# Kernel optimization log

Measured on AMD Instinct MI355X. Metric: run time of the kernel, lower is better.

## Reference

```python
import jax, jax.numpy as jnp
import numpy as np

B, H, W = 8, 448, 448
NUM_CLASSES, NUM_FEATURES = 80, 1280
TOPN, THRESHOLD = 4, 0.5


def conv(x, w, b, stride, pad):
    y = jax.lax.conv_general_dilated(x, w, (stride, stride), [(pad, pad), (pad, pad)],
                                     dimension_numbers=('NCHW', 'OIHW', 'NCHW'))
    return y + b[None, :, None, None]


def sample_bilinear(img, ys, xs):
    # img: [C, Hs, Ws]; ys: [oh] float coords; xs: [ow] float coords (align_corners=True grid)
    Hs, Ws = img.shape[1], img.shape[2]
    y0 = jnp.clip(jnp.floor(ys), 0.0, Hs - 1.0)
    x0 = jnp.clip(jnp.floor(xs), 0.0, Ws - 1.0)
    y0i = y0.astype(jnp.int32); y1i = jnp.minimum(y0i + 1, Hs - 1)
    x0i = x0.astype(jnp.int32); x1i = jnp.minimum(x0i + 1, Ws - 1)
    wy = (ys - y0)[:, None]   # [oh,1]
    wx = (xs - x0)[None, :]   # [1,ow]
    r0 = img[:, y0i, :]; r1 = img[:, y1i, :]          # [C,oh,Ws]
    a = r0[:, :, x0i]; b_ = r0[:, :, x1i]             # [C,oh,ow]
    c = r1[:, :, x0i]; d = r1[:, :, x1i]
    top = a * (1.0 - wx) + b_ * wx
    bot = c * (1.0 - wx) + d * wx
    return top * (1.0 - wy) + bot * wy


def minmax_norm(s):
    # torch: if max==min: s/max else (s-min)/(max-min); sigmoid output so max>0
    mn = s.min(-1, keepdims=True); mx = s.max(-1, keepdims=True)
    rng = mx - mn
    return jnp.where(rng > 0, (s - mn) / jnp.where(rng > 0, rng, 1.0),
                     s / jnp.where(mx != 0, mx, 1.0))


def obj_loc(score, threshold, dim):
    # first/last threshold crossing with min-size fallback (vectorized over leading dims)
    mask = score >= threshold
    any_ = mask.any(-1)
    first = jnp.argmax(mask, axis=-1)
    last = dim - jnp.argmax(mask[..., ::-1], axis=-1)   # exclusive
    lo = jnp.where(any_, first, int(dim * 0.125)).astype(jnp.int32)
    hi = jnp.where(any_, last, int(dim * 0.875)).astype(jnp.int32)
    minsize = int(np.ceil(dim * 0.125))
    need = jnp.maximum(minsize - (hi - lo), 0)
    lo = jnp.maximum(lo - (need + 1) // 2, 0)
    hi = jnp.minimum(hi + (need + 1) // 2, dim)
    return lo, hi


def one_crop(img, y1, y2, x1, x2):
    # crop img[:, y1:y2, x1:x2] and bilinearly resize to (H,W), align_corners=True
    oh, ow = img.shape[1], img.shape[2]
    ys = y1.astype(jnp.float32) + jnp.arange(oh, dtype=jnp.float32) * ((y2 - 1 - y1).astype(jnp.float32) / (oh - 1))
    xs = x1.astype(jnp.float32) + jnp.arange(ow, dtype=jnp.float32) * ((x2 - 1 - x1).astype(jnp.float32) / (ow - 1))
    return sample_bilinear(img, ys, xs)


def setup_inputs() -> dict:
    key = jax.random.key(0)
    k1, k2, k3 = jax.random.split(key, 3)
    return {
        'inputs': jax.random.normal(k1, (B, 3, H, W), dtype=jnp.float32),
        'feat_w': jax.random.normal(k2, (NUM_FEATURES, 3, 3, 3), dtype=jnp.float32) * 0.05,
        'feat_b': jnp.zeros((NUM_FEATURES,), dtype=jnp.float32),
        'cls_w': jax.random.normal(k3, (NUM_CLASSES, NUM_FEATURES, 1, 1), dtype=jnp.float32) * 0.02,
        'cls_b': jnp.zeros((NUM_CLASSES,), dtype=jnp.float32),
    }


def reference(inputs, feat_w, feat_b, cls_w, cls_b):
    b, c, h, w = inputs.shape
    # ---- backbone (stride-32 stand-in for MobileNetV2 features) ----
    ga = jnp.clip(conv(inputs, feat_w, feat_b, 32, 1), 0.0, 6.0)     # [b,1280,h/32,w/32]
    gf = ga.mean((2, 3), keepdims=True)                               # avg pool sh=h/32
    gs = jax.nn.sigmoid(conv(gf, cls_w, cls_b, 1, 0)).reshape(b, -1)  # [b,num_classes]
    # ---- CAM score path (on detached ga) ----
    cam = jax.nn.sigmoid(conv(jax.lax.stop_gradient(ga), cls_w, cls_b, 1, 0))
    ys_g = jnp.linspace(0.0, cam.shape[2] - 1.0, h)
    xs_g = jnp.linspace(0.0, cam.shape[3] - 1.0, w)
    cam_up = jax.vmap(lambda im: sample_bilinear(im, ys_g, xs_g))(cam)  # [b,C,h,w]
    wscore = cam_up.max(axis=2)   # max over height -> [b,C,w]
    hscore = cam_up.max(axis=3)   # max over width  -> [b,C,h]
    # ---- topN classes by global score ----
    _, topi = jax.lax.top_k(gs, TOPN)                                  # [b,topN]
    xs_s = jnp.take_along_axis(wscore, topi[:, :, None], axis=1)       # [b,topN,w]
    ys_s = jnp.take_along_axis(hscore, topi[:, :, None], axis=1)       # [b,topN,h]
    x1, x2 = obj_loc(minmax_norm(xs_s), THRESHOLD, w)
    y1, y2 = obj_loc(minmax_norm(ys_s), THRESHOLD, h)
    # ---- dynamic crop + bilinear resize, vectorized over (b, topN) ----
    crops = jax.vmap(lambda img, a1, a2, b1, b2:
                     jax.vmap(lambda p, q, r, s: one_crop(img, p, q, r, s))(a1, a2, b1, b2)
                     )(inputs, y1, y2, x1, x2)                          # [b,topN,3,h,w]
    li = jax.lax.stop_gradient(crops.reshape(b * TOPN, 3, h, w))
    la = jnp.clip(conv(li, feat_w, feat_b, 32, 1), 0.0, 6.0)
    lf = la.mean((2, 3), keepdims=True)
    ls = jax.nn.sigmoid(conv(lf, cls_w, cls_b, 1, 0)).reshape(b, TOPN, -1).max(axis=1)
    return gs, ls
```

## Files before the change

kernel.cpp:

```cpp
#include <hip/hip_runtime.h>
#include <math.h>

#define NB 8
#define TOPN 4
#define NC 80
#define NF 1280
#define HW 448
#define OS 14
#define NP 196
#define PATCH (3*42*42)
#define ROWPATCH (3*3*42)
#define WLDS (256*27)

__device__ __forceinline__ float sigmoidf_(float x) { return 1.0f / (1.0f + expf(-x)); }

__device__ __forceinline__ double wave_reduce_f64(double v) {
#pragma unroll
  for (int off = 32; off > 0; off >>= 1) v += __shfl_down(v, off);
  return v;
}

__global__ __launch_bounds__(256) void k1_conv_global(
    const float* __restrict__ in,
    const float* __restrict__ fw,
    const float* __restrict__ fb,
    float* __restrict__ ga,
    double* __restrict__ gfp)
{
  __shared__ float patch[ROWPATCH];
  __shared__ float wlds[WLDS];
  const int b = blockIdx.y, fc = blockIdx.x, oy = blockIdx.z, tid = threadIdx.x;
  for (int i = tid; i < WLDS; i += 256) wlds[i] = fw[fc * WLDS + i];
  for (int i = tid; i < ROWPATCH; i += 256) {
    int c = i / 126, rem = i % 126, rr = rem / 42, cc = rem % 42;
    int row = 32 * oy + rr - 1;
    int col = 32 * (cc / 3) + (cc % 3) - 1;
    float v = 0.0f;
    if (row >= 0 && col >= 0)
      v = in[((b * 3 + c) * HW + row) * HW + col];
    patch[i] = v;
  }
  __syncthreads();
  const int f = fc * 256 + tid;
  float w[27];
#pragma unroll
  for (int k = 0; k < 27; ++k) w[k] = wlds[tid * 27 + k];
  const float bias = fb[f];
  double sum = 0.0;
#pragma unroll 7
  for (int ox = 0; ox < OS; ++ox) {
    float acc = bias;
#pragma unroll
    for (int c = 0; c < 3; ++c)
#pragma unroll
      for (int ky = 0; ky < 3; ++ky)
#pragma unroll
        for (int kx = 0; kx < 3; ++kx)
          acc += patch[c * 126 + ky * 42 + ox * 3 + kx] * w[c * 9 + ky * 3 + kx];
    acc = fminf(fmaxf(acc, 0.0f), 6.0f);
    ga[((size_t)b * NP + oy * OS + ox) * NF + f] = acc;
    sum += (double)acc;
  }
  gfp[((size_t)oy * NB + b) * NF + f] = sum;
}

__global__ __launch_bounds__(1024) void k2_gs_topk(
    const double* __restrict__ gfp,
    const float* __restrict__ cw,
    const float* __restrict__ cb,
    float* __restrict__ gs_out,
    int* __restrict__ topi)
{
  __shared__ float gfs[NF];
  __shared__ float gsv[NC];
  const int b = blockIdx.x, tid = threadIdx.x;
  for (int i = tid; i < NF; i += 1024) {
    double s = 0.0;
#pragma unroll
    for (int z = 0; z < OS; ++z) s += gfp[((size_t)z * NB + b) * NF + i];
    gfs[i] = (float)(s / 196.0);
  }
  __syncthreads();
  const int wid = tid >> 6, lane = tid & 63;
  for (int j = 0; j < 5; ++j) {
    const int cls = wid * 5 + j;
    const float* w = cw + (size_t)cls * NF;
    double acc = 0.0;
#pragma unroll
    for (int k = 0; k < NF / 64; ++k) {
      int f = k * 64 + lane;
      acc += (double)w[f] * (double)gfs[f];
    }
    acc = wave_reduce_f64(acc);
    if (lane == 0) {
      float s = sigmoidf_((float)(acc + (double)cb[cls]));
      gsv[cls] = s;
      gs_out[b * NC + cls] = s;
    }
  }
  __syncthreads();
  if (wid == 0) {
    float v0 = gsv[lane];
    float v1 = (lane < NC - 64) ? gsv[64 + lane] : -1e30f;
    const int i0 = lane, i1 = 64 + lane;
#pragma unroll
    for (int t = 0; t < TOPN; ++t) {
      float bv; int bi;
      if (v1 > v0) { bv = v1; bi = i1; } else { bv = v0; bi = i0; }
#pragma unroll
      for (int off = 1; off < 64; off <<= 1) {
        float ov = __shfl_xor(bv, off);
        int oi = __shfl_xor(bi, off);
        if (ov > bv || (ov == bv && oi < bi)) { bv = ov; bi = oi; }
      }
      if (lane == 0) topi[b * TOPN + t] = bi;
      if (bi == i0) v0 = -1e30f;
      if (bi == i1) v1 = -1e30f;
    }
  }
}

__global__ __launch_bounds__(256) void k3a_cam(
    const float* __restrict__ ga,
    const float* __restrict__ cw,
    const float* __restrict__ cb,
    const int* __restrict__ topi,
    float* __restrict__ camg)
{
  __shared__ float clsw[NF];
  const int pc = blockIdx.x, bt = blockIdx.y;
  const int tid = threadIdx.x, wid = tid >> 6, lane = tid & 63;
  const int p = pc * 4 + wid;
  const int b = bt >> 2;
  const int cls = topi[bt];
  for (int i = tid; i < NF; i += 256) clsw[i] = cw[(size_t)cls * NF + i];
  __syncthreads();
  const float* g = ga + ((size_t)b * NP + p) * NF;
  double acc = 0.0;
#pragma unroll
  for (int k = 0; k < NF / 64; ++k) {
    const int f = k * 64 + lane;
    acc += (double)g[f] * (double)clsw[f];
  }
  acc = wave_reduce_f64(acc);
  if (lane == 0) camg[bt * NP + p] = sigmoidf_((float)(acc + (double)cb[cls]));
}

__global__ __launch_bounds__(256) void k3b_bounds_stage(
    const float* __restrict__ camg,
    const float* __restrict__ in,
    float* __restrict__ patchg)
{
  __shared__ float cam[NP];
  __shared__ float wsS[HW];
  __shared__ float hsS[HW];
  __shared__ int jlo[OS], jhi[OS];
  __shared__ int shb[4];
  const int bt = blockIdx.x, tid = threadIdx.x;
  const int wid = tid >> 6, lane = tid & 63;
  const float SC = 13.0f / 447.0f;

  if (tid < OS) { jlo[tid] = 1 << 30; jhi[tid] = -1; }
  for (int i = tid; i < NP; i += 256) cam[i] = camg[bt * NP + i];
  __syncthreads();
  for (int j = tid; j < HW; j += 256) {
    float yp = (float)j * SC;
    int y0 = (int)floorf(yp); if (y0 > 13) y0 = 13;
    atomicMin(&jlo[y0], j);
    atomicMax(&jhi[y0], j);
  }
  __syncthreads();

  for (int x = tid; x < HW; x += 256) {
    float xp = (float)x * SC;
    int x0 = (int)floorf(xp); if (x0 > 13) x0 = 13;
    float wx = xp - (float)x0;
    int x1i = min(x0 + 1, 13);
    {
      float cv[OS];
#pragma unroll
      for (int r = 0; r < OS; ++r)
        cv[r] = cam[r * OS + x0] * (1.0f - wx) + cam[r * OS + x1i] * wx;
      float m = -1e30f;
#pragma unroll
      for (int r = 0; r < OS; ++r) {
        int jl = jlo[r], jh = jhi[r];
        if (jl <= jh) {
          const int rn = (r + 1 < OS) ? r + 1 : OS - 1;
          float yp1 = (float)jl * SC; float wy1 = yp1 - (float)r;
          float yp2 = (float)jh * SC; float wy2 = yp2 - (float)r;
          float v1 = cv[r] * (1.0f - wy1) + cv[rn] * wy1;
          float v2 = cv[r] * (1.0f - wy2) + cv[rn] * wy2;
          m = fmaxf(m, fmaxf(v1, v2));
        }
      }
      wsS[x] = m;
    }
    {
      float cv[OS];
#pragma unroll
      for (int c = 0; c < OS; ++c)
        cv[c] = cam[x0 * OS + c] * (1.0f - wx) + cam[x1i * OS + c] * wx;
      float m = -1e30f;
#pragma unroll
      for (int r = 0; r < OS; ++r) {
        int jl = jlo[r], jh = jhi[r];
        if (jl <= jh) {
          const int rn = (r + 1 < OS) ? r + 1 : OS - 1;
          float xp1 = (float)jl * SC; float w1 = xp1 - (float)r;
          float xp2 = (float)jh * SC; float w2 = xp2 - (float)r;
          float v1 = cv[r] * (1.0f - w1) + cv[rn] * w1;
          float v2 = cv[r] * (1.0f - w2) + cv[rn] * w2;
          m = fmaxf(m, fmaxf(v1, v2));
        }
      }
      hsS[x] = m;
    }
  }
  __syncthreads();

  if (wid < 2) {
    const float* s = (wid == 0) ? wsS : hsS;
    float v[7];
    float mn = 1e30f, mx = -1e30f;
#pragma unroll
    for (int q = 0; q < 7; ++q) {
      v[q] = s[lane + 64 * q];
      mn = fminf(mn, v[q]); mx = fmaxf(mx, v[q]);
    }
#pragma unroll
    for (int off = 32; off > 0; off >>= 1) {
      mn = fminf(mn, __shfl_down(mn, off));
      mx = fmaxf(mx, __shfl_down(mx, off));
    }
    mn = __shfl(mn, 0); mx = __shfl(mx, 0);
    float rng = mx - mn;
    float dnm = (mx != 0.0f) ? mx : 1.0f;
    int firstL = 1 << 30, lastL = -1;
#pragma unroll
    for (int q = 0; q < 7; ++q) {
      float nv = (rng > 0.0f) ? (v[q] - mn) / rng : v[q] / dnm;
      if (nv >= 0.5f) {
        int idx = lane + 64 * q;
        firstL = min(firstL, idx);
        lastL = max(lastL, idx);
      }
    }
#pragma unroll
    for (int off = 32; off > 0; off >>= 1) {
      firstL = min(firstL, __shfl_down(firstL, off));
      lastL = max(lastL, __shfl_down(lastL, off));
    }
    if (lane == 0) {
      int lo, hi;
      if (lastL >= 0) { lo = firstL; hi = lastL + 1; }
      else { lo = 56; hi = 392; }
      int need = 56 - (hi - lo); if (need < 0) need = 0;
      int pad = (need + 1) >> 1;
      lo = lo - pad; if (lo < 0) lo = 0;
      hi = hi + pad; if (hi > HW) hi = HW;
      if (wid == 0) { shb[2] = lo; shb[3] = hi; }
      else          { shb[0] = lo; shb[1] = hi; }
    }
  }
  __syncthreads();

  const int b = bt >> 2;
  const int y1 = shb[0], y2 = shb[1], x1 = shb[2], x2 = shb[3];
  const float y1f = (float)y1, x1f = (float)x1;
  const float sy = (float)(y2 - 1 - y1) / 447.0f;
  const float sx = (float)(x2 - 1 - x1) / 447.0f;
  const float* img = in + (size_t)b * 3 * HW * HW;
  for (int i = tid; i < PATCH; i += 256) {
    int c = i / 1764, rem = i % 1764, r = rem / 42, cc = rem % 42;
    int yy = 32 * (r / 3) + (r % 3) - 1;
    int xx = 32 * (cc / 3) + (cc % 3) - 1;
    float v = 0.0f;
    if (yy >= 0 && xx >= 0) {
      float ys = y1f + (float)yy * sy;
      float xs = x1f + (float)xx * sx;
      float y0 = floorf(ys); if (y0 < 0.0f) y0 = 0.0f; if (y0 > 447.0f) y0 = 447.0f;
      float x0 = floorf(xs); if (x0 < 0.0f) x0 = 0.0f; if (x0 > 447.0f) x0 = 447.0f;
      int y0i = (int)y0, x0i = (int)x0;
      int y1i = min(y0i + 1, HW - 1), x1i = min(x0i + 1, HW - 1);
      float wy = ys - y0, wx = xs - x0;
      const float* ic = img + (size_t)c * HW * HW;
      float a  = ic[y0i * HW + x0i], bb = ic[y0i * HW + x1i];
      float cc2 = ic[y1i * HW + x0i], d  = ic[y1i * HW + x1i];
      float top = a * (1.0f - wx) + bb * wx;
      float bot = cc2 * (1.0f - wx) + d * wx;
      v = top * (1.0f - wy) + bot * wy;
    }
    patchg[(size_t)bt * PATCH + i] = v;
  }
}

__global__ __launch_bounds__(256) void k4_conv_local(
    const float* __restrict__ patchg,
    const float* __restrict__ fw,
    const float* __restrict__ fb,
    double* __restrict__ lfp)
{
  __shared__ float patch[ROWPATCH];
  __shared__ float wlds[WLDS];
  const int bt = blockIdx.y, fc = blockIdx.x, oy = blockIdx.z, tid = threadIdx.x;
  for (int i = tid; i < WLDS; i += 256) wlds[i] = fw[fc * WLDS + i];
  for (int i = tid; i < ROWPATCH; i += 256) {
    int c = i / 126, rem = i % 126, rr = rem / 42, cc = rem % 42;
    patch[i] = patchg[(size_t)bt * PATCH + c * 1764 + (3 * oy + rr) * 42 + cc];
  }
  __syncthreads();
  const int f = fc * 256 + tid;
  float w[27];
#pragma unroll
  for (int k = 0; k < 27; ++k) w[k] = wlds[tid * 27 + k];
  const float bias = fb[f];
  double sum = 0.0;
#pragma unroll 7
  for (int ox = 0; ox < OS; ++ox) {
    float acc = bias;
#pragma unroll
    for (int c = 0; c < 3; ++c)
#pragma unroll
      for (int ky = 0; ky < 3; ++ky)
#pragma unroll
        for (int kx = 0; kx < 3; ++kx)
          acc += patch[c * 126 + ky * 42 + ox * 3 + kx] * w[c * 9 + ky * 3 + kx];
    acc = fminf(fmaxf(acc, 0.0f), 6.0f);
    sum += (double)acc;
  }
  lfp[((size_t)oy * (NB * TOPN) + bt) * NF + f] = sum;
}

__global__ __launch_bounds__(256) void kcomb_lf(
    const double* __restrict__ lfp,
    float* __restrict__ lf32)
{
  const int j = blockIdx.x * 256 + threadIdx.x;
  double s = 0.0;
#pragma unroll
  for (int z = 0; z < OS; ++z) s += lfp[(size_t)z * 40960 + j];
  lf32[j] = (float)(s / 196.0);
}

__global__ __launch_bounds__(64) void k5_ls(
    const float* __restrict__ lf32,
    const float* __restrict__ cw,
    const float* __restrict__ cb,
    float* __restrict__ ls_out)
{
  const int cls = blockIdx.x, b = blockIdx.y, lane = threadIdx.x;
  const float* w = cw + (size_t)cls * NF;
  const float* l0 = lf32 + (size_t)(b * TOPN + 0) * NF;
  const float* l1 = lf32 + (size_t)(b * TOPN + 1) * NF;
  const float* l2 = lf32 + (size_t)(b * TOPN + 2) * NF;
  const float* l3 = lf32 + (size_t)(b * TOPN + 3) * NF;
  double a0 = 0.0, a1 = 0.0, a2 = 0.0, a3 = 0.0;
#pragma unroll
  for (int k = 0; k < NF / 64; ++k) {
    const int f = k * 64 + lane;
    const double wv = (double)w[f];
    a0 += wv * (double)l0[f];
    a1 += wv * (double)l1[f];
    a2 += wv * (double)l2[f];
    a3 += wv * (double)l3[f];
  }
  a0 = wave_reduce_f64(a0);
  a1 = wave_reduce_f64(a1);
  a2 = wave_reduce_f64(a2);
  a3 = wave_reduce_f64(a3);
  if (lane == 0) {
    const double bias = (double)cb[cls];
    float m = sigmoidf_((float)(a0 + bias));
    m = fmaxf(m, sigmoidf_((float)(a1 + bias)));
    m = fmaxf(m, sigmoidf_((float)(a2 + bias)));
    m = fmaxf(m, sigmoidf_((float)(a3 + bias)));
    ls_out[b * NC + cls] = m;
  }
}

extern "C" void kernel_launch(void* const* d_in, const int* in_sizes, int n_in,
                              void* d_out, int out_size, void* d_ws, size_t ws_size,
                              hipStream_t stream) {
  const float* in = (const float*)d_in[0];
  const float* fw = (const float*)d_in[1];
  const float* fb = (const float*)d_in[2];
  const float* cw = (const float*)d_in[3];
  const float* cb = (const float*)d_in[4];
  float* out = (float*)d_out;

  double* gfp = (double*)d_ws;
  double* lfp = gfp + (size_t)OS * NB * NF;
  float* ga = (float*)(lfp + (size_t)OS * NB * TOPN * NF);
  float* lf32 = ga + (size_t)NB * NP * NF;
  float* patchg = lf32 + (size_t)NB * TOPN * NF;
  float* camg = patchg + (size_t)NB * TOPN * PATCH;
  int* topi = (int*)(camg + NB * TOPN * NP);

  k1_conv_global<<<dim3(5, NB, OS), 256, 0, stream>>>(in, fw, fb, ga, gfp);
  k2_gs_topk<<<NB, 1024, 0, stream>>>(gfp, cw, cb, out, topi);
  k3a_cam<<<dim3(NP / 4, NB * TOPN), 256, 0, stream>>>(ga, cw, cb, topi, camg);
  k3b_bounds_stage<<<NB * TOPN, 256, 0, stream>>>(camg, in, patchg);
  k4_conv_local<<<dim3(5, NB * TOPN, OS), 256, 0, stream>>>(patchg, fw, fb, lfp);
  kcomb_lf<<<NB * TOPN * NF / 256, 256, 0, stream>>>(lfp, lf32);
  k5_ls<<<dim3(NC, NB), 64, 0, stream>>>(lf32, cw, cb, out + 640);
}
```

Measured before the change: 144.6 us.

## Fuse CAM and bounds kernels; replace partial-sum combine with double atomics

Merges the CAM dot-product kernel into the bounds/staging kernel, which now runs at 1024 threads per block and has each wave compute four CAM positions at once. It also drops the separate combine kernel: the local-conv kernel now atomically adds its per-row double sums into a zeroed accumulator, and the final kernel applies the mean scaling on read. Together this cuts two launches and the intermediate CAM and partial-sum buffers. The cost is only 32 blocks for the CAM work instead of 1568, plus contention on the double atomics, whose summation order is no longer deterministic.

```diff
diff --git a/kernel.cpp b/kernel.cpp
--- a/kernel.cpp
+++ b/kernel.cpp
@@ -120,37 +120,16 @@
   }
 }
 
-__global__ __launch_bounds__(256) void k3a_cam(
+__global__ __launch_bounds__(1024) void k3_cam_bounds_stage(
     const float* __restrict__ ga,
     const float* __restrict__ cw,
     const float* __restrict__ cb,
     const int* __restrict__ topi,
-    float* __restrict__ camg)
+    const float* __restrict__ in,
+    float* __restrict__ patchg,
+    double* __restrict__ lfa)
 {
   __shared__ float clsw[NF];
-  const int pc = blockIdx.x, bt = blockIdx.y;
-  const int tid = threadIdx.x, wid = tid >> 6, lane = tid & 63;
-  const int p = pc * 4 + wid;
-  const int b = bt >> 2;
-  const int cls = topi[bt];
-  for (int i = tid; i < NF; i += 256) clsw[i] = cw[(size_t)cls * NF + i];
-  __syncthreads();
-  const float* g = ga + ((size_t)b * NP + p) * NF;
-  double acc = 0.0;
-#pragma unroll
-  for (int k = 0; k < NF / 64; ++k) {
-    const int f = k * 64 + lane;
-    acc += (double)g[f] * (double)clsw[f];
-  }
-  acc = wave_reduce_f64(acc);
-  if (lane == 0) camg[bt * NP + p] = sigmoidf_((float)(acc + (double)cb[cls]));
-}
-
-__global__ __launch_bounds__(256) void k3b_bounds_stage(
-    const float* __restrict__ camg,
-    const float* __restrict__ in,
-    float* __restrict__ patchg)
-{
   __shared__ float cam[NP];
   __shared__ float wsS[HW];
   __shared__ float hsS[HW];
@@ -158,12 +137,42 @@
   __shared__ int shb[4];
   const int bt = blockIdx.x, tid = threadIdx.x;
   const int wid = tid >> 6, lane = tid & 63;
+  const int b = bt >> 2;
+  const int cls = topi[bt];
   const float SC = 13.0f / 447.0f;
 
   if (tid < OS) { jlo[tid] = 1 << 30; jhi[tid] = -1; }
-  for (int i = tid; i < NP; i += 256) cam[i] = camg[bt * NP + i];
-  __syncthreads();
-  for (int j = tid; j < HW; j += 256) {
+  for (int i = tid; i < NF; i += 1024) clsw[i] = cw[(size_t)cls * NF + i];
+  for (int i = tid; i < NF; i += 1024) lfa[(size_t)bt * NF + i] = 0.0;
+  __syncthreads();
+
+  const double bias = (double)cb[cls];
+  for (int p0 = wid; p0 < NP; p0 += 64) {
+    double a[4] = {0.0, 0.0, 0.0, 0.0};
+    const float* g[4];
+    int pv[4];
+#pragma unroll
+    for (int s = 0; s < 4; ++s) {
+      int p = p0 + 16 * s;
+      pv[s] = (p < NP) ? p : -1;
+      g[s] = ga + ((size_t)b * NP + ((p < NP) ? p : 0)) * NF;
+    }
+#pragma unroll
+    for (int k = 0; k < NF / 64; ++k) {
+      const int f = k * 64 + lane;
+      const double wv = (double)clsw[f];
+#pragma unroll
+      for (int s = 0; s < 4; ++s) a[s] += (double)g[s][f] * wv;
+    }
+#pragma unroll
+    for (int s = 0; s < 4; ++s) {
+      a[s] = wave_reduce_f64(a[s]);
+      if (lane == 0 && pv[s] >= 0) cam[pv[s]] = sigmoidf_((float)(a[s] + bias));
+    }
+  }
+  __syncthreads();
+
+  for (int j = tid; j < HW; j += 1024) {
     float yp = (float)j * SC;
     int y0 = (int)floorf(yp); if (y0 > 13) y0 = 13;
     atomicMin(&jlo[y0], j);
@@ -171,7 +180,7 @@
   }
   __syncthreads();
 
-  for (int x = tid; x < HW; x += 256) {
+  for (int x = tid; x < HW; x += 1024) {
     float xp = (float)x * SC;
     int x0 = (int)floorf(xp); if (x0 > 13) x0 = 13;
     float wx = xp - (float)x0;
@@ -265,13 +274,12 @@
   }
   __syncthreads();
 
-  const int b = bt >> 2;
   const int y1 = shb[0], y2 = shb[1], x1 = shb[2], x2 = shb[3];
   const float y1f = (float)y1, x1f = (float)x1;
   const float sy = (float)(y2 - 1 - y1) / 447.0f;
   const float sx = (float)(x2 - 1 - x1) / 447.0f;
   const float* img = in + (size_t)b * 3 * HW * HW;
-  for (int i = tid; i < PATCH; i += 256) {
+  for (int i = tid; i < PATCH; i += 1024) {
     int c = i / 1764, rem = i % 1764, r = rem / 42, cc = rem % 42;
     int yy = 32 * (r / 3) + (r % 3) - 1;
     int xx = 32 * (cc / 3) + (cc % 3) - 1;
@@ -299,7 +307,7 @@
     const float* __restrict__ patchg,
     const float* __restrict__ fw,
     const float* __restrict__ fb,
-    double* __restrict__ lfp)
+    double* __restrict__ lfa)
 {
   __shared__ float patch[ROWPATCH];
   __shared__ float wlds[WLDS];
@@ -329,41 +337,30 @@
     acc = fminf(fmaxf(acc, 0.0f), 6.0f);
     sum += (double)acc;
   }
-  lfp[((size_t)oy * (NB * TOPN) + bt) * NF + f] = sum;
-}
-
-__global__ __launch_bounds__(256) void kcomb_lf(
-    const double* __restrict__ lfp,
-    float* __restrict__ lf32)
-{
-  const int j = blockIdx.x * 256 + threadIdx.x;
-  double s = 0.0;
-#pragma unroll
-  for (int z = 0; z < OS; ++z) s += lfp[(size_t)z * 40960 + j];
-  lf32[j] = (float)(s / 196.0);
+  atomicAdd(&lfa[(size_t)bt * NF + f], sum);
 }
 
 __global__ __launch_bounds__(64) void k5_ls(
-    const float* __restrict__ lf32,
+    const double* __restrict__ lfa,
     const float* __restrict__ cw,
     const float* __restrict__ cb,
     float* __restrict__ ls_out)
 {
   const int cls = blockIdx.x, b = blockIdx.y, lane = threadIdx.x;
   const float* w = cw + (size_t)cls * NF;
-  const float* l0 = lf32 + (size_t)(b * TOPN + 0) * NF;
-  const float* l1 = lf32 + (size_t)(b * TOPN + 1) * NF;
-  const float* l2 = lf32 + (size_t)(b * TOPN + 2) * NF;
-  const float* l3 = lf32 + (size_t)(b * TOPN + 3) * NF;
+  const double* l0 = lfa + (size_t)(b * TOPN + 0) * NF;
+  const double* l1 = lfa + (size_t)(b * TOPN + 1) * NF;
+  const double* l2 = lfa + (size_t)(b * TOPN + 2) * NF;
+  const double* l3 = lfa + (size_t)(b * TOPN + 3) * NF;
   double a0 = 0.0, a1 = 0.0, a2 = 0.0, a3 = 0.0;
 #pragma unroll
   for (int k = 0; k < NF / 64; ++k) {
     const int f = k * 64 + lane;
     const double wv = (double)w[f];
-    a0 += wv * (double)l0[f];
-    a1 += wv * (double)l1[f];
-    a2 += wv * (double)l2[f];
-    a3 += wv * (double)l3[f];
+    a0 += wv * (double)(float)(l0[f] / 196.0);
+    a1 += wv * (double)(float)(l1[f] / 196.0);
+    a2 += wv * (double)(float)(l2[f] / 196.0);
+    a3 += wv * (double)(float)(l3[f] / 196.0);
   }
   a0 = wave_reduce_f64(a0);
   a1 = wave_reduce_f64(a1);
@@ -390,18 +387,14 @@
   float* out = (float*)d_out;
 
   double* gfp = (double*)d_ws;
-  double* lfp = gfp + (size_t)OS * NB * NF;
-  float* ga = (float*)(lfp + (size_t)OS * NB * TOPN * NF);
-  float* lf32 = ga + (size_t)NB * NP * NF;
-  float* patchg = lf32 + (size_t)NB * TOPN * NF;
-  float* camg = patchg + (size_t)NB * TOPN * PATCH;
-  int* topi = (int*)(camg + NB * TOPN * NP);
+  double* lfa = gfp + (size_t)OS * NB * NF;
+  float* ga = (float*)(lfa + (size_t)NB * TOPN * NF);
+  float* patchg = ga + (size_t)NB * NP * NF;
+  int* topi = (int*)(patchg + (size_t)NB * TOPN * PATCH);
 
   k1_conv_global<<<dim3(5, NB, OS), 256, 0, stream>>>(in, fw, fb, ga, gfp);
   k2_gs_topk<<<NB, 1024, 0, stream>>>(gfp, cw, cb, out, topi);
-  k3a_cam<<<dim3(NP / 4, NB * TOPN), 256, 0, stream>>>(ga, cw, cb, topi, camg);
-  k3b_bounds_stage<<<NB * TOPN, 256, 0, stream>>>(camg, in, patchg);
-  k4_conv_local<<<dim3(5, NB * TOPN, OS), 256, 0, stream>>>(patchg, fw, fb, lfp);
-  kcomb_lf<<<NB * TOPN * NF / 256, 256, 0, stream>>>(lfp, lf32);
-  k5_ls<<<dim3(NC, NB), 64, 0, stream>>>(lf32, cw, cb, out + 640);
-}
+  k3_cam_bounds_stage<<<NB * TOPN, 1024, 0, stream>>>(ga, cw, cb, topi, in, patchg, lfa);
+  k4_conv_local<<<dim3(5, NB * TOPN, OS), 256, 0, stream>>>(patchg, fw, fb, lfa);
+  k5_ls<<<dim3(NC, NB), 64, 0, stream>>>(lfa, cw, cb, out + 640);
+}
```

Measured after the change: 172.0 us. 1.19x slower.
